# Kernel tuning notes

Measured on AMD Instinct MI355X. Metric: run time of the kernel, lower is better.

The kernel has to match this reference:

```python
import jax, jax.numpy as jnp
import numpy as np

NUM_GRAPHS = 512   # number of graphs in the batch
MAX_NODES = 192    # static pad bound (actual sizes are in [96,160])
TOTAL = 65536      # total atoms across all graphs
D = 256            # model dim (from MultiheadAttention(256, 4))
H = 4              # heads
DH = D // H        # head dim = 64


def setup_inputs() -> dict:
    # Ragged graph sizes that sum exactly to TOTAL (pairs 128+p / 128-p).
    rng = np.random.default_rng(0)
    p = rng.integers(0, 33, size=NUM_GRAPHS // 2)
    sizes = np.concatenate([128 + p, 128 - p])
    rng.shuffle(sizes)
    batch = np.repeat(np.arange(NUM_GRAPHS, dtype=np.int32), sizes)

    key = jax.random.key(0)
    ks = jax.random.split(key, 12)
    s = 0.02
    return {
        "x": jax.random.normal(ks[0], (TOTAL, D), jnp.float32),
        "batch": jnp.asarray(batch),
        # attn1 (torch MultiheadAttention packed in_proj + out_proj)
        "in_w1": jax.random.normal(ks[1], (3 * D, D), jnp.float32) * s,
        "in_b1": jnp.zeros((3 * D,), jnp.float32),
        "out_w1": jax.random.normal(ks[2], (D, D), jnp.float32) * s,
        "out_b1": jnp.zeros((D,), jnp.float32),
        # attn2
        "in_w2": jax.random.normal(ks[3], (3 * D, D), jnp.float32) * s,
        "in_b2": jnp.zeros((3 * D,), jnp.float32),
        "out_w2": jax.random.normal(ks[4], (D, D), jnp.float32) * s,
        "out_b2": jnp.zeros((D,), jnp.float32),
        # readout MLP: 256 -> 256 -> 128 -> 1 (dropout is identity in eval)
        "r_w1": jax.random.normal(ks[5], (256, 256), jnp.float32) * s,
        "r_b1": jnp.zeros((256,), jnp.float32),
        "r_w2": jax.random.normal(ks[6], (128, 256), jnp.float32) * s,
        "r_b2": jnp.zeros((128,), jnp.float32),
        "r_w3": jax.random.normal(ks[7], (1, 128), jnp.float32) * s,
        "r_b3": jnp.zeros((1,), jnp.float32),
    }


def _mha(xd, mask, in_w, in_b, out_w, out_b):
    # xd: [B, L, D], mask: [B, L] (True = valid key). torch MHA semantics.
    B, L, _ = xd.shape
    qkv = xd @ in_w.T + in_b                                  # [B, L, 3D]
    q, k, v = jnp.split(qkv, 3, axis=-1)
    split = lambda t: t.reshape(B, L, H, DH).transpose(0, 2, 1, 3)  # [B,H,L,DH]
    q, k, v = split(q), split(k), split(v)
    scores = jnp.einsum("bhqd,bhkd->bhqk", q, k) / jnp.sqrt(jnp.float32(DH))
    scores = jnp.where(mask[:, None, None, :], scores, -jnp.inf)
    attn = jax.nn.softmax(scores, axis=-1)                    # each graph has >=1 node
    o = jnp.einsum("bhqk,bhkd->bhqd", attn, v)                # [B,H,L,DH]
    o = o.transpose(0, 2, 1, 3).reshape(B, L, D)
    return o @ out_w.T + out_b


def reference(x, batch, in_w1, in_b1, out_w1, out_b1,
              in_w2, in_b2, out_w2, out_b2,
              r_w1, r_b1, r_w2, r_b2, r_w3, r_b3):
    # Scatter ragged atoms into a padded dense [B, MAX_NODES, D] block
    # (equivalent to the per-graph Python loop, but one fused pass).
    idx = jnp.arange(TOTAL)
    pos = idx - jnp.searchsorted(batch, batch, side="left")   # position within graph
    dense = jnp.zeros((NUM_GRAPHS, MAX_NODES, D), x.dtype).at[batch, pos].set(x)
    mask = jnp.zeros((NUM_GRAPHS, MAX_NODES), bool).at[batch, pos].set(True)

    h = _mha(dense, mask, in_w1, in_b1, out_w1, out_b1)
    h = _mha(h, mask, in_w2, in_b2, out_w2, out_b2)

    # masked mean-pool over valid nodes of each graph
    m = mask[..., None].astype(h.dtype)
    pooled = (h * m).sum(axis=1) / m.sum(axis=1)              # [B, D]

    h1 = jax.nn.relu(pooled @ r_w1.T + r_b1)                  # dropout = identity (eval)
    h2 = jax.nn.relu(h1 @ r_w2.T + r_b2)
    energy = h2 @ r_w3.T + r_b3                               # [B, 1]
    return energy[:, 0]                                       # (batch_size,)
```

## Files before the change

kernel.cpp:

```cpp
#include <hip/hip_runtime.h>
#include <math.h>

#define TOTAL 65536
#define NG 512
#define DMODEL 256
#define QKVLD 768

typedef __attribute__((ext_vector_type(8))) short bf16x8;
typedef __attribute__((ext_vector_type(4))) float f32x4;

__device__ inline ushort f2bf(float f) {
    unsigned int u = __float_as_uint(f);
    unsigned int r = (u + 0x7FFFu + ((u >> 16) & 1u)) >> 16;
    return (ushort)r;
}
__device__ inline float bf2f(ushort h) { return __uint_as_float(((unsigned int)h) << 16); }

__device__ __forceinline__ void llds16(const void* gptr, void* lptr) {
    __builtin_amdgcn_global_load_lds(
        (const __attribute__((address_space(1))) unsigned int*)gptr,
        (__attribute__((address_space(3))) unsigned int*)lptr, 16, 0, 0);
}

__global__ __launch_bounds__(256) void prep_kernel(
    const float* __restrict__ x, const float* __restrict__ in_w1,
    const float* __restrict__ in_w2, const float* __restrict__ out_w1,
    const float* __restrict__ out_b1, const float* __restrict__ in_b2,
    const int* __restrict__ batch,
    ushort* __restrict__ xb, ushort* __restrict__ Wb1,
    ushort* __restrict__ Wc2b, float* __restrict__ bc2, int* __restrict__ starts)
{
    const int b = blockIdx.x, t = threadIdx.x;
    if (b < 16384) {
        int i = b * 256 + t;
        float4 v = ((const float4*)x)[i];
        ushort4 u;
        u.x = f2bf(v.x); u.y = f2bf(v.y); u.z = f2bf(v.z); u.w = f2bf(v.w);
        ((ushort4*)xb)[i] = u;
    } else if (b < 16576) {
        int i = (b - 16384) * 256 + t;
        float4 v = ((const float4*)in_w1)[i];
        ushort4 u;
        u.x = f2bf(v.x); u.y = f2bf(v.y); u.z = f2bf(v.z); u.w = f2bf(v.w);
        ((ushort4*)Wb1)[i] = u;
    } else if (b < 17344) {
        const int n = b - 16576;
        __shared__ float wrow[256];
        wrow[t] = in_w2[n * 256 + t];
        __syncthreads();
        float s = 0.f;
#pragma unroll 8
        for (int j = 0; j < 256; ++j) s += wrow[j] * out_w1[j * 256 + t];
        Wc2b[n * 256 + t] = f2bf(s);
    } else if (b < 17347) {
        int n = (b - 17344) * 256 + t;
        if (n < 768) {
            float s = 0.f;
            for (int j = 0; j < 256; ++j) s += in_w2[n * 256 + j] * out_b1[j];
            bc2[n] = s + in_b2[n];
        }
    } else {
        int g = (b - 17347) * 256 + t;
        if (g < NG) {
            int lo = 0, hi = TOTAL;
            while (lo < hi) {
                int mid = (lo + hi) >> 1;
                if (batch[mid] < g) lo = mid + 1; else hi = mid;
            }
            starts[g] = lo;
            if (g == 0) starts[NG] = TOTAL;
        }
    }
}

__global__ __launch_bounds__(256) void gemm_mfma(
    const ushort* __restrict__ A,
    const ushort* __restrict__ W,
    const float* __restrict__ bias,
    ushort* __restrict__ C, int ldc)
{
    __shared__ ushort As[128 * 64];
    __shared__ ushort Bs[128 * 64];
    const int tid = threadIdx.x;
    const int lane = tid & 63, wid = tid >> 6;
    const int grp = lane >> 4, ln16 = lane & 15;
    const int wm = wid & 1, wn = wid >> 1;
    const int n0 = blockIdx.x * 128, m0 = blockIdx.y * 128;

    const int lrow = lane >> 3;
    const int lchunk = (lane & 7) ^ lrow;

    f32x4 acc[4][4];
#pragma unroll
    for (int i = 0; i < 4; ++i)
#pragma unroll
        for (int j = 0; j < 4; ++j) acc[i][j] = (f32x4){0.f, 0.f, 0.f, 0.f};

    for (int k0 = 0; k0 < 256; k0 += 64) {
#pragma unroll
        for (int j = 0; j < 4; ++j) {
            int band = wid * 32 + j * 8;
            int row = band + lrow;
            llds16(A + (size_t)(m0 + row) * 256 + k0 + lchunk * 8, &As[band * 64]);
            llds16(W + (size_t)(n0 + row) * 256 + k0 + lchunk * 8, &Bs[band * 64]);
        }
        __syncthreads();
#pragma unroll
        for (int kc = 0; kc < 2; ++kc) {
            bf16x8 a[4], b[4];
#pragma unroll
            for (int i = 0; i < 4; ++i) {
                int r = wm * 64 + i * 16 + ln16;
                int p = (kc * 4 + grp) ^ (r & 7);
                a[i] = *(const bf16x8*)&As[r * 64 + p * 8];
            }
#pragma unroll
            for (int j = 0; j < 4; ++j) {
                int r = wn * 64 + j * 16 + ln16;
                int p = (kc * 4 + grp) ^ (r & 7);
                b[j] = *(const bf16x8*)&Bs[r * 64 + p * 8];
            }
#pragma unroll
            for (int i = 0; i < 4; ++i)
#pragma unroll
                for (int j = 0; j < 4; ++j)
                    acc[i][j] = __builtin_amdgcn_mfma_f32_16x16x32_bf16(a[i], b[j], acc[i][j], 0, 0, 0);
        }
        __syncthreads();
    }

#pragma unroll
    for (int j = 0; j < 4; ++j) {
        int col = n0 + wn * 64 + j * 16 + ln16;
        float bv = bias[col];
#pragma unroll
        for (int i = 0; i < 4; ++i) {
            int r0 = m0 + wm * 64 + i * 16 + grp * 4;
#pragma unroll
            for (int reg = 0; reg < 4; ++reg)
                C[(size_t)(r0 + reg) * ldc + col] = f2bf(acc[i][j][reg] + bv);
        }
    }
}

#define VLD 168
#define PLD 72

__global__ __launch_bounds__(256) void attn_mfma(const ushort* __restrict__ qkv,
                                                 ushort* __restrict__ obuf,
                                                 float* __restrict__ psumOut,
                                                 const int* __restrict__ starts) {
    __shared__ ushort Ks[160 * 64];
    __shared__ ushort Vt[64 * VLD];
    __shared__ ushort Ps[4 * 16 * PLD];
    __shared__ float  red[4][64];
    const int g = blockIdx.x;
    const int h = blockIdx.y;
    int s = starts[g];
    int e = starts[g + 1];
    s = (s < 0) ? 0 : ((s > TOTAL) ? TOTAL : s);
    e = (e < s) ? s : ((e > TOTAL) ? TOTAL : e);
    int L = e - s;
    if (L > 160) L = 160;
    if (L < 1) L = 1;
    const int tid = threadIdx.x;
    const int lane = tid & 63, wid = tid >> 6;
    const int grp = lane >> 4, ln16 = lane & 15;
    const int lrow = lane >> 3;
    const int lchunk = (lane & 7) ^ lrow;

#pragma unroll
    for (int r = 0; r < 5; ++r) {
        int band = (r * 4 + wid) * 8;
        int row = band + lrow;
        int crow = (row < L) ? row : (L - 1);
        llds16(qkv + (size_t)(s + crow) * QKVLD + 256 + h * 64 + lchunk * 8, &Ks[band * 64]);
    }
#pragma unroll
    for (int r = 0; r < 5; ++r) {
        int idx = r * 256 + tid;
        int kc = idx >> 6;
        int d = idx & 63;
        ushort tmp[8];
#pragma unroll
        for (int j = 0; j < 8; ++j) {
            int key = kc * 8 + j;
            int ckey = (key < L) ? key : (L - 1);
            tmp[j] = qkv[(size_t)(s + ckey) * QKVLD + 512 + h * 64 + d];
        }
        *(uint4*)&Vt[d * VLD + kc * 8] = *(const uint4*)tmp;
    }
    __syncthreads();

    ushort* myP = &Ps[wid * 16 * PLD];
    float psum[4] = {0.f, 0.f, 0.f, 0.f};
    const bool pooled = (psumOut != nullptr);

    for (int q0 = wid * 16; q0 < L; q0 += 64) {
        bf16x8 qa[2];
        {
            int qi = q0 + ln16;
            int grow = (qi < L) ? (s + qi) : s;
            const ushort* qbase = qkv + (size_t)grow * QKVLD + h * 64;
            qa[0] = *(const bf16x8*)(qbase + grp * 8);
            qa[1] = *(const bf16x8*)(qbase + 32 + grp * 8);
        }
        f32x4 sc[10];
#pragma unroll
        for (int kt = 0; kt < 10; ++kt) {
            int row = kt * 16 + ln16;
            int p0 = grp ^ (row & 7);
            int p1 = (4 + grp) ^ (row & 7);
            bf16x8 b0 = *(const bf16x8*)&Ks[row * 64 + p0 * 8];
            bf16x8 b1 = *(const bf16x8*)&Ks[row * 64 + p1 * 8];
            f32x4 z = (f32x4){0.f, 0.f, 0.f, 0.f};
            z = __builtin_amdgcn_mfma_f32_16x16x32_bf16(qa[0], b0, z, 0, 0, 0);
            z = __builtin_amdgcn_mfma_f32_16x16x32_bf16(qa[1], b1, z, 0, 0, 0);
            sc[kt] = z;
        }
        float sm[4] = {0.f, 0.f, 0.f, 0.f};
#pragma unroll
        for (int kt = 0; kt < 10; ++kt) {
            bool dead = (kt * 16 + ln16) >= L;
#pragma unroll
            for (int r = 0; r < 4; ++r) {
                float p = __expf(dead ? -INFINITY : sc[kt][r] * 0.125f);
                sc[kt][r] = p;
                sm[r] += p;
            }
        }
#pragma unroll
        for (int m = 1; m <= 8; m <<= 1)
#pragma unroll
            for (int r = 0; r < 4; ++r) sm[r] += __shfl_xor(sm[r], m, 64);
        float inv[4];
#pragma unroll
        for (int r = 0; r < 4; ++r) inv[r] = 1.f / sm[r];

        f32x4 o[4];
#pragma unroll
        for (int dt = 0; dt < 4; ++dt) o[dt] = (f32x4){0.f, 0.f, 0.f, 0.f};
#pragma unroll
        for (int st = 0; st < 3; ++st) {
            const int nkt = (st == 2) ? 2 : 4;
            const int nkc = (st == 2) ? 1 : 2;
#pragma unroll
            for (int kti = 0; kti < 4; ++kti) {
                if (kti < nkt) {
                    int kt = st * 4 + kti;
#pragma unroll
                    for (int r = 0; r < 4; ++r)
                        myP[(grp * 4 + r) * PLD + kti * 16 + ln16] = f2bf(sc[kt][r]);
                }
            }
#pragma unroll
            for (int kc2 = 0; kc2 < 2; ++kc2) {
                if (kc2 < nkc) {
                    bf16x8 pa = *(const bf16x8*)&myP[ln16 * PLD + kc2 * 32 + grp * 8];
                    int kcg = st * 2 + kc2;
#pragma unroll
                    for (int dt = 0; dt < 4; ++dt) {
                        bf16x8 vb = *(const bf16x8*)&Vt[(dt * 16 + ln16) * VLD + kcg * 32 + grp * 8];
                        o[dt] = __builtin_amdgcn_mfma_f32_16x16x32_bf16(pa, vb, o[dt], 0, 0, 0);
                    }
                }
            }
        }
        if (pooled) {
#pragma unroll
            for (int dt = 0; dt < 4; ++dt)
#pragma unroll
                for (int reg = 0; reg < 4; ++reg) {
                    int q = q0 + grp * 4 + reg;
                    if (q < L) psum[dt] += o[dt][reg] * inv[reg];
                }
        } else {
#pragma unroll
            for (int dt = 0; dt < 4; ++dt)
#pragma unroll
                for (int reg = 0; reg < 4; ++reg) {
                    int q = q0 + grp * 4 + reg;
                    if (q < L)
                        obuf[(size_t)(s + q) * DMODEL + h * 64 + dt * 16 + ln16] =
                            f2bf(o[dt][reg] * inv[reg]);
                }
        }
    }

    if (pooled) {
#pragma unroll
        for (int dt = 0; dt < 4; ++dt) {
            psum[dt] += __shfl_xor(psum[dt], 16, 64);
            psum[dt] += __shfl_xor(psum[dt], 32, 64);
        }
        if (grp == 0) {
#pragma unroll
            for (int dt = 0; dt < 4; ++dt) red[wid][dt * 16 + ln16] = psum[dt];
        }
        __syncthreads();
        if (tid < 64) {
            float v = red[0][tid] + red[1][tid] + red[2][tid] + red[3][tid];
            psumOut[g * DMODEL + h * 64 + tid] = v;
        }
    }
}

__global__ __launch_bounds__(256) void readout_kernel(
    const float* __restrict__ psum, const int* __restrict__ starts,
    const float* __restrict__ ow2, const float* __restrict__ ob2,
    const float* __restrict__ w1, const float* __restrict__ b1,
    const float* __restrict__ w2, const float* __restrict__ b2,
    const float* __restrict__ w3, const float* __restrict__ b3,
    float* __restrict__ out)
{
    __shared__ float xs[256], ps[256], h1s[256], h2s[128];
    const int g = blockIdx.x, t = threadIdx.x;
    int s = starts[g], e = starts[g + 1];
    s = (s < 0) ? 0 : ((s > TOTAL) ? TOTAL : s);
    e = (e < s) ? s : ((e > TOTAL) ? TOTAL : e);
    int L = e - s;
    if (L < 1) L = 1;
    xs[t] = psum[g * 256 + t] / (float)L;
    __syncthreads();
    {
        const float* wr = ow2 + t * 256;
        float s0 = 0.f;
#pragma unroll 8
        for (int i = 0; i < 256; ++i) s0 += xs[i] * wr[i];
        ps[t] = s0 + ob2[t];
    }
    __syncthreads();
    {
        const float* wr = w1 + t * 256;
        float s0 = 0.f;
#pragma unroll 8
        for (int i = 0; i < 256; ++i) s0 += ps[i] * wr[i];
        float v = s0 + b1[t];
        h1s[t] = v > 0.f ? v : 0.f;
    }
    __syncthreads();
    if (t < 128) {
        const float* wr = w2 + t * 256;
        float s0 = 0.f;
#pragma unroll 8
        for (int i = 0; i < 256; ++i) s0 += h1s[i] * wr[i];
        float v = s0 + b2[t];
        h2s[t] = v > 0.f ? v : 0.f;
    }
    __syncthreads();
    if (t < 64) {
        float v = h2s[t] * w3[t] + h2s[t + 64] * w3[t + 64];
#pragma unroll
        for (int off = 32; off > 0; off >>= 1) v += __shfl_down(v, off, 64);
        if (t == 0) out[g] = v + b3[0];
    }
}

__global__ __launch_bounds__(256) void zero_out_kernel(float* __restrict__ out, int n) {
    int i = blockIdx.x * 256 + threadIdx.x;
    if (i < n) out[i] = 0.f;
}

extern "C" void kernel_launch(void* const* d_in, const int* in_sizes, int n_in,
                              void* d_out, int out_size, void* d_ws, size_t ws_size,
                              hipStream_t stream) {
    float* out = (float*)d_out;

    const int expect[16] = {
        TOTAL * DMODEL, TOTAL,
        3 * DMODEL * DMODEL, 3 * DMODEL,
        DMODEL * DMODEL, DMODEL,
        3 * DMODEL * DMODEL, 3 * DMODEL,
        DMODEL * DMODEL, DMODEL,
        256 * 256, 256,
        128 * 256, 128,
        128, 1
    };
    const size_t NEEDED = 135536640ull;
    bool ok = (n_in == 16) && (out_size == NG) && (d_ws != nullptr) && (ws_size >= NEEDED);
    if (ok) {
        for (int i = 0; i < 16; ++i)
            if (in_sizes[i] != expect[i]) { ok = false; break; }
    }
    if (!ok) {
        zero_out_kernel<<<(out_size + 255) / 256, 256, 0, stream>>>(out, out_size);
        return;
    }

    const float* x      = (const float*)d_in[0];
    const int*   batch  = (const int*)d_in[1];
    const float* in_w1  = (const float*)d_in[2];
    const float* in_b1  = (const float*)d_in[3];
    const float* out_w1 = (const float*)d_in[4];
    const float* out_b1 = (const float*)d_in[5];
    const float* in_w2  = (const float*)d_in[6];
    const float* in_b2  = (const float*)d_in[7];
    const float* out_w2 = (const float*)d_in[8];
    const float* out_b2 = (const float*)d_in[9];
    const float* r_w1   = (const float*)d_in[10];
    const float* r_b1   = (const float*)d_in[11];
    const float* r_w2   = (const float*)d_in[12];
    const float* r_b2   = (const float*)d_in[13];
    const float* r_w3   = (const float*)d_in[14];
    const float* r_b3   = (const float*)d_in[15];

    char* ws = (char*)d_ws;
    int*    starts = (int*)(ws + 0);
    float*  bc2    = (float*)(ws + 4096);
    float*  psum   = (float*)(ws + 8192);
    ushort* Wc2b   = (ushort*)(ws + 532480);
    ushort* Wb1    = (ushort*)(ws + 925696);
    ushort* bufO   = (ushort*)(ws + 1318912);
    ushort* bufQKV = (ushort*)(ws + 34873344ull);

    prep_kernel<<<17349, 256, 0, stream>>>(x, in_w1, in_w2, out_w1, out_b1, in_b2,
                                           batch, bufO, Wb1, Wc2b, bc2, starts);

    gemm_mfma<<<dim3(6, 512), 256, 0, stream>>>(bufO, Wb1, in_b1, bufQKV, QKVLD);
    attn_mfma<<<dim3(NG, 4), 256, 0, stream>>>(bufQKV, bufO, nullptr, starts);

    gemm_mfma<<<dim3(6, 512), 256, 0, stream>>>(bufO, Wc2b, bc2, bufQKV, QKVLD);
    attn_mfma<<<dim3(NG, 4), 256, 0, stream>>>(bufQKV, bufO, psum, starts);

    readout_kernel<<<NG, 256, 0, stream>>>(psum, starts, out_w2, out_b2,
                                           r_w1, r_b1, r_w2, r_b2, r_w3, r_b3, out);
}
```

Baseline: 377.0 us.

## Fuse QKV projection GEMM into per-graph attention kernel

Replaces the separate QKV GEMM and attention kernels with one kernel per (graph, head). It computes the head's Q, K and V projections from the input rows in shared memory and then runs attention directly. This removes the QKV intermediate buffer's global write and read and cuts the number of launches. In exchange, each block recomputes projections on a small tile (at most 160 rows) with less data reuse, uses more shared memory per block, and the phases are serialized inside the block.

```diff
diff --git a/kernel.cpp b/kernel.cpp
--- a/kernel.cpp
+++ b/kernel.cpp
@@ -73,87 +73,17 @@
     }
 }
 
-__global__ __launch_bounds__(256) void gemm_mfma(
-    const ushort* __restrict__ A,
+#define VLD 168
+
+__global__ __launch_bounds__(256) void fused_layer(
+    const ushort* __restrict__ X,
     const ushort* __restrict__ W,
     const float* __restrict__ bias,
-    ushort* __restrict__ C, int ldc)
+    ushort* __restrict__ obuf,
+    float* __restrict__ psumOut,
+    const int* __restrict__ starts)
 {
-    __shared__ ushort As[128 * 64];
-    __shared__ ushort Bs[128 * 64];
-    const int tid = threadIdx.x;
-    const int lane = tid & 63, wid = tid >> 6;
-    const int grp = lane >> 4, ln16 = lane & 15;
-    const int wm = wid & 1, wn = wid >> 1;
-    const int n0 = blockIdx.x * 128, m0 = blockIdx.y * 128;
-
-    const int lrow = lane >> 3;
-    const int lchunk = (lane & 7) ^ lrow;
-
-    f32x4 acc[4][4];
-#pragma unroll
-    for (int i = 0; i < 4; ++i)
-#pragma unroll
-        for (int j = 0; j < 4; ++j) acc[i][j] = (f32x4){0.f, 0.f, 0.f, 0.f};
-
-    for (int k0 = 0; k0 < 256; k0 += 64) {
-#pragma unroll
-        for (int j = 0; j < 4; ++j) {
-            int band = wid * 32 + j * 8;
-            int row = band + lrow;
-            llds16(A + (size_t)(m0 + row) * 256 + k0 + lchunk * 8, &As[band * 64]);
-            llds16(W + (size_t)(n0 + row) * 256 + k0 + lchunk * 8, &Bs[band * 64]);
-        }
-        __syncthreads();
-#pragma unroll
-        for (int kc = 0; kc < 2; ++kc) {
-            bf16x8 a[4], b[4];
-#pragma unroll
-            for (int i = 0; i < 4; ++i) {
-                int r = wm * 64 + i * 16 + ln16;
-                int p = (kc * 4 + grp) ^ (r & 7);
-                a[i] = *(const bf16x8*)&As[r * 64 + p * 8];
-            }
-#pragma unroll
-            for (int j = 0; j < 4; ++j) {
-                int r = wn * 64 + j * 16 + ln16;
-                int p = (kc * 4 + grp) ^ (r & 7);
-                b[j] = *(const bf16x8*)&Bs[r * 64 + p * 8];
-            }
-#pragma unroll
-            for (int i = 0; i < 4; ++i)
-#pragma unroll
-                for (int j = 0; j < 4; ++j)
-                    acc[i][j] = __builtin_amdgcn_mfma_f32_16x16x32_bf16(a[i], b[j], acc[i][j], 0, 0, 0);
-        }
-        __syncthreads();
-    }
-
-#pragma unroll
-    for (int j = 0; j < 4; ++j) {
-        int col = n0 + wn * 64 + j * 16 + ln16;
-        float bv = bias[col];
-#pragma unroll
-        for (int i = 0; i < 4; ++i) {
-            int r0 = m0 + wm * 64 + i * 16 + grp * 4;
-#pragma unroll
-            for (int reg = 0; reg < 4; ++reg)
-                C[(size_t)(r0 + reg) * ldc + col] = f2bf(acc[i][j][reg] + bv);
-        }
-    }
-}
-
-#define VLD 168
-#define PLD 72
-
-__global__ __launch_bounds__(256) void attn_mfma(const ushort* __restrict__ qkv,
-                                                 ushort* __restrict__ obuf,
-                                                 float* __restrict__ psumOut,
-                                                 const int* __restrict__ starts) {
-    __shared__ ushort Ks[160 * 64];
-    __shared__ ushort Vt[64 * VLD];
-    __shared__ ushort Ps[4 * 16 * PLD];
-    __shared__ float  red[4][64];
+    __shared__ __align__(16) ushort smem[26112];
     const int g = blockIdx.x;
     const int h = blockIdx.y;
     int s = starts[g];
@@ -166,128 +96,249 @@
     const int tid = threadIdx.x;
     const int lane = tid & 63, wid = tid >> 6;
     const int grp = lane >> 4, ln16 = lane & 15;
-    const int lrow = lane >> 3;
-    const int lchunk = (lane & 7) ^ lrow;
-
-#pragma unroll
-    for (int r = 0; r < 5; ++r) {
-        int band = (r * 4 + wid) * 8;
-        int row = band + lrow;
-        int crow = (row < L) ? row : (L - 1);
-        llds16(qkv + (size_t)(s + crow) * QKVLD + 256 + h * 64 + lchunk * 8, &Ks[band * 64]);
-    }
-#pragma unroll
-    for (int r = 0; r < 5; ++r) {
-        int idx = r * 256 + tid;
-        int kc = idx >> 6;
-        int d = idx & 63;
-        ushort tmp[8];
-#pragma unroll
-        for (int j = 0; j < 8; ++j) {
-            int key = kc * 8 + j;
-            int ckey = (key < L) ? key : (L - 1);
-            tmp[j] = qkv[(size_t)(s + ckey) * QKVLD + 512 + h * 64 + d];
-        }
-        *(uint4*)&Vt[d * VLD + kc * 8] = *(const uint4*)tmp;
-    }
+    const int lrow8 = lane >> 3;
+    const int lxor = (lane & 7) ^ lrow8;
+    const int nt = (wid < 2) ? 3 : 2;
+    const int mt0 = (wid < 2) ? wid * 3 : 6 + (wid - 2) * 2;
+    const int Sw = 20992 + wid * 1152;
+
+    float bq[4], bk[4], bv2[2];
+#pragma unroll
+    for (int j = 0; j < 4; ++j) {
+        bq[j] = bias[h * 64 + j * 16 + ln16];
+        bk[j] = bias[256 + h * 64 + j * 16 + ln16];
+    }
+    const int wm = wid & 1, wn = wid >> 1;
+#pragma unroll
+    for (int j = 0; j < 2; ++j)
+        bv2[j] = bias[512 + h * 64 + wn * 32 + j * 16 + ln16];
+
+    f32x4 acc[3][8];
+#pragma unroll
+    for (int t = 0; t < 3; ++t)
+#pragma unroll
+        for (int j = 0; j < 8; ++j) acc[t][j] = (f32x4){0.f, 0.f, 0.f, 0.f};
+
+    for (int c = 0; c < 4; ++c) {
+#pragma unroll
+        for (int r = 0; r < 5; ++r) {
+            int band = wid * 5 + r;
+            int row = band * 8 + lrow8;
+            int crow = (row < L) ? row : (L - 1);
+            llds16(X + (size_t)(s + crow) * 256 + c * 64 + lxor * 8, &smem[band * 512]);
+        }
+#pragma unroll
+        for (int r = 0; r < 4; ++r) {
+            int band = wid * 4 + r;
+            int gg = band * 8 + lrow8;
+            int wrow = (gg < 64) ? (h * 64 + gg) : (256 + h * 64 + (gg - 64));
+            llds16(W + (size_t)wrow * 256 + c * 64 + lxor * 8, &smem[10240 + band * 512]);
+        }
+        __syncthreads();
+#pragma unroll
+        for (int kc = 0; kc < 2; ++kc) {
+            bf16x8 a[3], bb[8];
+#pragma unroll
+            for (int t = 0; t < 3; ++t) {
+                if (t < nt) {
+                    int row = (mt0 + t) * 16 + ln16;
+                    a[t] = *(const bf16x8*)&smem[row * 64 + (((kc * 4 + grp) ^ (row & 7)) * 8)];
+                }
+            }
+#pragma unroll
+            for (int j = 0; j < 8; ++j) {
+                int col = j * 16 + ln16;
+                bb[j] = *(const bf16x8*)&smem[10240 + col * 64 + (((kc * 4 + grp) ^ (col & 7)) * 8)];
+            }
+#pragma unroll
+            for (int t = 0; t < 3; ++t) {
+                if (t < nt) {
+#pragma unroll
+                    for (int j = 0; j < 8; ++j)
+                        acc[t][j] = __builtin_amdgcn_mfma_f32_16x16x32_bf16(a[t], bb[j], acc[t][j], 0, 0, 0);
+                }
+            }
+        }
+        __syncthreads();
+    }
+#pragma unroll
+    for (int t = 0; t < 3; ++t) {
+        if (t < nt) {
+#pragma unroll
+            for (int j = 0; j < 4; ++j) {
+                int d = j * 16 + ln16;
+#pragma unroll
+                for (int reg = 0; reg < 4; ++reg) {
+                    int key = (mt0 + t) * 16 + grp * 4 + reg;
+                    smem[key * 64 + (((d >> 3) ^ (key & 7)) * 8) + (d & 7)] =
+                        f2bf(acc[t][4 + j][reg] + bk[j]);
+                }
+            }
+        }
+    }
+
+    f32x4 accv[5][2];
+#pragma unroll
+    for (int i = 0; i < 5; ++i)
+#pragma unroll
+        for (int j = 0; j < 2; ++j) accv[i][j] = (f32x4){0.f, 0.f, 0.f, 0.f};
+
+    for (int c = 0; c < 4; ++c) {
+#pragma unroll
+        for (int r = 0; r < 5; ++r) {
+            int band = wid * 5 + r;
+            int row = band * 8 + lrow8;
+            int crow = (row < L) ? row : (L - 1);
+            llds16(X + (size_t)(s + crow) * 256 + c * 64 + lxor * 8, &smem[10240 + band * 512]);
+        }
+#pragma unroll
+        for (int r = 0; r < 2; ++r) {
+            int band = wid * 2 + r;
+            int gg = band * 8 + lrow8;
+            llds16(W + (size_t)(512 + h * 64 + gg) * 256 + c * 64 + lxor * 8,
+                   &smem[20992 + band * 512]);
+        }
+        __syncthreads();
+#pragma unroll
+        for (int kc = 0; kc < 2; ++kc) {
+            bf16x8 av[5], bv[2];
+#pragma unroll
+            for (int i = 0; i < 5; ++i) {
+                int row = (wm * 5 + i) * 16 + ln16;
+                av[i] = *(const bf16x8*)&smem[10240 + row * 64 + (((kc * 4 + grp) ^ (row & 7)) * 8)];
+            }
+#pragma unroll
+            for (int j = 0; j < 2; ++j) {
+                int col = wn * 32 + j * 16 + ln16;
+                bv[j] = *(const bf16x8*)&smem[20992 + col * 64 + (((kc * 4 + grp) ^ (col & 7)) * 8)];
+            }
+#pragma unroll
+            for (int i = 0; i < 5; ++i)
+#pragma unroll
+                for (int j = 0; j < 2; ++j)
+                    accv[i][j] = __builtin_amdgcn_mfma_f32_16x16x32_bf16(av[i], bv[j], accv[i][j], 0, 0, 0);
+        }
+        __syncthreads();
+    }
+#pragma unroll
+    for (int i = 0; i < 5; ++i)
+#pragma unroll
+        for (int j = 0; j < 2; ++j) {
+            int d = wn * 32 + j * 16 + ln16;
+            int keybase = wm * 80 + i * 16 + grp * 4;
+            ushort4 pk;
+            pk.x = f2bf(accv[i][j][0] + bv2[j]);
+            pk.y = f2bf(accv[i][j][1] + bv2[j]);
+            pk.z = f2bf(accv[i][j][2] + bv2[j]);
+            pk.w = f2bf(accv[i][j][3] + bv2[j]);
+            *(ushort4*)&smem[10240 + d * VLD + keybase] = pk;
+        }
     __syncthreads();
 
-    ushort* myP = &Ps[wid * 16 * PLD];
     float psum[4] = {0.f, 0.f, 0.f, 0.f};
     const bool pooled = (psumOut != nullptr);
 
-    for (int q0 = wid * 16; q0 < L; q0 += 64) {
-        bf16x8 qa[2];
-        {
-            int qi = q0 + ln16;
-            int grow = (qi < L) ? (s + qi) : s;
-            const ushort* qbase = qkv + (size_t)grow * QKVLD + h * 64;
-            qa[0] = *(const bf16x8*)(qbase + grp * 8);
-            qa[1] = *(const bf16x8*)(qbase + 32 + grp * 8);
-        }
-        f32x4 sc[10];
-#pragma unroll
-        for (int kt = 0; kt < 10; ++kt) {
-            int row = kt * 16 + ln16;
-            int p0 = grp ^ (row & 7);
-            int p1 = (4 + grp) ^ (row & 7);
-            bf16x8 b0 = *(const bf16x8*)&Ks[row * 64 + p0 * 8];
-            bf16x8 b1 = *(const bf16x8*)&Ks[row * 64 + p1 * 8];
-            f32x4 z = (f32x4){0.f, 0.f, 0.f, 0.f};
-            z = __builtin_amdgcn_mfma_f32_16x16x32_bf16(qa[0], b0, z, 0, 0, 0);
-            z = __builtin_amdgcn_mfma_f32_16x16x32_bf16(qa[1], b1, z, 0, 0, 0);
-            sc[kt] = z;
-        }
-        float sm[4] = {0.f, 0.f, 0.f, 0.f};
-#pragma unroll
-        for (int kt = 0; kt < 10; ++kt) {
-            bool dead = (kt * 16 + ln16) >= L;
-#pragma unroll
-            for (int r = 0; r < 4; ++r) {
-                float p = __expf(dead ? -INFINITY : sc[kt][r] * 0.125f);
-                sc[kt][r] = p;
-                sm[r] += p;
-            }
-        }
-#pragma unroll
-        for (int m = 1; m <= 8; m <<= 1)
-#pragma unroll
-            for (int r = 0; r < 4; ++r) sm[r] += __shfl_xor(sm[r], m, 64);
-        float inv[4];
-#pragma unroll
-        for (int r = 0; r < 4; ++r) inv[r] = 1.f / sm[r];
-
-        f32x4 o[4];
-#pragma unroll
-        for (int dt = 0; dt < 4; ++dt) o[dt] = (f32x4){0.f, 0.f, 0.f, 0.f};
-#pragma unroll
-        for (int st = 0; st < 3; ++st) {
-            const int nkt = (st == 2) ? 2 : 4;
-            const int nkc = (st == 2) ? 1 : 2;
-#pragma unroll
-            for (int kti = 0; kti < 4; ++kti) {
-                if (kti < nkt) {
-                    int kt = st * 4 + kti;
-#pragma unroll
-                    for (int r = 0; r < 4; ++r)
-                        myP[(grp * 4 + r) * PLD + kti * 16 + ln16] = f2bf(sc[kt][r]);
-                }
-            }
-#pragma unroll
-            for (int kc2 = 0; kc2 < 2; ++kc2) {
-                if (kc2 < nkc) {
-                    bf16x8 pa = *(const bf16x8*)&myP[ln16 * PLD + kc2 * 32 + grp * 8];
-                    int kcg = st * 2 + kc2;
-#pragma unroll
-                    for (int dt = 0; dt < 4; ++dt) {
-                        bf16x8 vb = *(const bf16x8*)&Vt[(dt * 16 + ln16) * VLD + kcg * 32 + grp * 8];
-                        o[dt] = __builtin_amdgcn_mfma_f32_16x16x32_bf16(pa, vb, o[dt], 0, 0, 0);
+#pragma unroll
+    for (int t = 0; t < 3; ++t) {
+        if (t < nt) {
+            int q0 = (mt0 + t) * 16;
+            if (q0 < L) {
+#pragma unroll
+                for (int j = 0; j < 4; ++j)
+#pragma unroll
+                    for (int reg = 0; reg < 4; ++reg) {
+                        int q = grp * 4 + reg;
+                        int d = j * 16 + ln16;
+                        smem[Sw + q * 64 + (((d >> 3) ^ (q & 7)) * 8) + (d & 7)] =
+                            f2bf(acc[t][j][reg] + bq[j]);
                     }
-                }
-            }
-        }
-        if (pooled) {
-#pragma unroll
-            for (int dt = 0; dt < 4; ++dt)
-#pragma unroll
-                for (int reg = 0; reg < 4; ++reg) {
-                    int q = q0 + grp * 4 + reg;
-                    if (q < L) psum[dt] += o[dt][reg] * inv[reg];
-                }
-        } else {
-#pragma unroll
-            for (int dt = 0; dt < 4; ++dt)
-#pragma unroll
-                for (int reg = 0; reg < 4; ++reg) {
-                    int q = q0 + grp * 4 + reg;
-                    if (q < L)
-                        obuf[(size_t)(s + q) * DMODEL + h * 64 + dt * 16 + ln16] =
-                            f2bf(o[dt][reg] * inv[reg]);
-                }
+                bf16x8 qa0 = *(const bf16x8*)&smem[Sw + ln16 * 64 + ((grp ^ (ln16 & 7)) * 8)];
+                bf16x8 qa1 = *(const bf16x8*)&smem[Sw + ln16 * 64 + (((4 + grp) ^ (ln16 & 7)) * 8)];
+
+                f32x4 sc[10];
+#pragma unroll
+                for (int kt = 0; kt < 10; ++kt) {
+                    int row = kt * 16 + ln16;
+                    bf16x8 b0 = *(const bf16x8*)&smem[row * 64 + ((grp ^ (row & 7)) * 8)];
+                    bf16x8 b1 = *(const bf16x8*)&smem[row * 64 + (((4 + grp) ^ (row & 7)) * 8)];
+                    f32x4 z = (f32x4){0.f, 0.f, 0.f, 0.f};
+                    z = __builtin_amdgcn_mfma_f32_16x16x32_bf16(qa0, b0, z, 0, 0, 0);
+                    z = __builtin_amdgcn_mfma_f32_16x16x32_bf16(qa1, b1, z, 0, 0, 0);
+                    sc[kt] = z;
+                }
+                float sm[4] = {0.f, 0.f, 0.f, 0.f};
+#pragma unroll
+                for (int kt = 0; kt < 10; ++kt) {
+                    bool dead = (kt * 16 + ln16) >= L;
+#pragma unroll
+                    for (int r = 0; r < 4; ++r) {
+                        float p = __expf(dead ? -INFINITY : sc[kt][r] * 0.125f);
+                        sc[kt][r] = p;
+                        sm[r] += p;
+                    }
+                }
+#pragma unroll
+                for (int m = 1; m <= 8; m <<= 1)
+#pragma unroll
+                    for (int r = 0; r < 4; ++r) sm[r] += __shfl_xor(sm[r], m, 64);
+                float inv[4];
+#pragma unroll
+                for (int r = 0; r < 4; ++r) inv[r] = 1.f / sm[r];
+
+                f32x4 o[4];
+#pragma unroll
+                for (int dt = 0; dt < 4; ++dt) o[dt] = (f32x4){0.f, 0.f, 0.f, 0.f};
+#pragma unroll
+                for (int st = 0; st < 3; ++st) {
+                    const int nkt = (st == 2) ? 2 : 4;
+                    const int nkc = (st == 2) ? 1 : 2;
+#pragma unroll
+                    for (int kti = 0; kti < 4; ++kti) {
+                        if (kti < nkt) {
+                            int kt = st * 4 + kti;
+#pragma unroll
+                            for (int r = 0; r < 4; ++r)
+                                smem[Sw + (grp * 4 + r) * 72 + kti * 16 + ln16] = f2bf(sc[kt][r]);
+                        }
+                    }
+#pragma unroll
+                    for (int kc2 = 0; kc2 < 2; ++kc2) {
+                        if (kc2 < nkc) {
+                            bf16x8 pa = *(const bf16x8*)&smem[Sw + ln16 * 72 + kc2 * 32 + grp * 8];
+                            int kcg = st * 2 + kc2;
+#pragma unroll
+                            for (int dt = 0; dt < 4; ++dt) {
+                                bf16x8 vb = *(const bf16x8*)&smem[10240 + (dt * 16 + ln16) * VLD + kcg * 32 + grp * 8];
+                                o[dt] = __builtin_amdgcn_mfma_f32_16x16x32_bf16(pa, vb, o[dt], 0, 0, 0);
+                            }
+                        }
+                    }
+                }
+                if (pooled) {
+#pragma unroll
+                    for (int dt = 0; dt < 4; ++dt)
+#pragma unroll
+                        for (int reg = 0; reg < 4; ++reg) {
+                            int q = q0 + grp * 4 + reg;
+                            if (q < L) psum[dt] += o[dt][reg] * inv[reg];
+                        }
+                } else {
+#pragma unroll
+                    for (int dt = 0; dt < 4; ++dt)
+#pragma unroll
+                        for (int reg = 0; reg < 4; ++reg) {
+                            int q = q0 + grp * 4 + reg;
+                            if (q < L)
+                                obuf[(size_t)(s + q) * DMODEL + h * 64 + dt * 16 + ln16] =
+                                    f2bf(o[dt][reg] * inv[reg]);
+                        }
+                }
+            }
         }
     }
 
     if (pooled) {
+        float* redf = (float*)&smem[25600];
 #pragma unroll
         for (int dt = 0; dt < 4; ++dt) {
             psum[dt] += __shfl_xor(psum[dt], 16, 64);
@@ -295,11 +346,11 @@
         }
         if (grp == 0) {
 #pragma unroll
-            for (int dt = 0; dt < 4; ++dt) red[wid][dt * 16 + ln16] = psum[dt];
+            for (int dt = 0; dt < 4; ++dt) redf[wid * 64 + dt * 16 + ln16] = psum[dt];
         }
         __syncthreads();
         if (tid < 64) {
-            float v = red[0][tid] + red[1][tid] + red[2][tid] + red[3][tid];
+            float v = redf[tid] + redf[64 + tid] + redf[128 + tid] + redf[192 + tid];
             psumOut[g * DMODEL + h * 64 + tid] = v;
         }
     }
@@ -410,17 +461,14 @@
     float*  psum   = (float*)(ws + 8192);
     ushort* Wc2b   = (ushort*)(ws + 532480);
     ushort* Wb1    = (ushort*)(ws + 925696);
-    ushort* bufO   = (ushort*)(ws + 1318912);
-    ushort* bufQKV = (ushort*)(ws + 34873344ull);
+    ushort* xb     = (ushort*)(ws + 1318912);
+    ushort* bufO1  = (ushort*)(ws + 34873344ull);
 
     prep_kernel<<<17349, 256, 0, stream>>>(x, in_w1, in_w2, out_w1, out_b1, in_b2,
-                                           batch, bufO, Wb1, Wc2b, bc2, starts);
-
-    gemm_mfma<<<dim3(6, 512), 256, 0, stream>>>(bufO, Wb1, in_b1, bufQKV, QKVLD);
-    attn_mfma<<<dim3(NG, 4), 256, 0, stream>>>(bufQKV, bufO, nullptr, starts);
-
-    gemm_mfma<<<dim3(6, 512), 256, 0, stream>>>(bufO, Wc2b, bc2, bufQKV, QKVLD);
-    attn_mfma<<<dim3(NG, 4), 256, 0, stream>>>(bufQKV, bufO, psum, starts);
+                                           batch, xb, Wb1, Wc2b, bc2, starts);
+
+    fused_layer<<<dim3(NG, 4), 256, 0, stream>>>(xb, Wb1, in_b1, bufO1, nullptr, starts);
+    fused_layer<<<dim3(NG, 4), 256, 0, stream>>>(bufO1, Wc2b, bc2, nullptr, psum, starts);
 
     readout_kernel<<<NG, 256, 0, stream>>>(psum, starts, out_w2, out_b2,
                                            r_w1, r_b1, r_w2, r_b2, r_w3, r_b3, out);
```

Result: slower. 450.6 us (+19.5%).

## Fuse all stages into one persistent cooperative kernel with grid syncs

Applied to the files above, without the earlier changes.

Refactors the prep, QKV GEMM, attention and readout kernels into device functions and runs them as job loops inside a single cooperative mega-kernel of 768 blocks separated by grid-wide syncs. This removes the separate kernel launches and inter-kernel gaps. It adds grid barrier costs, caps occupancy at three blocks per CU with shared memory sized for the largest stage, and may worsen load balance. A fallback to the original multi-launch path runs if the cooperative launch fails.

```diff
diff --git a/kernel.cpp b/kernel.cpp
--- a/kernel.cpp
+++ b/kernel.cpp
@@ -1,10 +1,15 @@
 #include <hip/hip_runtime.h>
+#include <hip/hip_cooperative_groups.h>
 #include <math.h>
+
+namespace cg = cooperative_groups;
 
 #define TOTAL 65536
 #define NG 512
 #define DMODEL 256
 #define QKVLD 768
+#define VLD 168
+#define PLD 72
 
 typedef __attribute__((ext_vector_type(8))) short bf16x8;
 typedef __attribute__((ext_vector_type(4))) float f32x4;
@@ -22,15 +27,17 @@
         (__attribute__((address_space(3))) unsigned int*)lptr, 16, 0, 0);
 }
 
-__global__ __launch_bounds__(256) void prep_kernel(
+
+__device__ __forceinline__ void prep_job(
+    int b, int t,
     const float* __restrict__ x, const float* __restrict__ in_w1,
     const float* __restrict__ in_w2, const float* __restrict__ out_w1,
     const float* __restrict__ out_b1, const float* __restrict__ in_b2,
     const int* __restrict__ batch,
     ushort* __restrict__ xb, ushort* __restrict__ Wb1,
-    ushort* __restrict__ Wc2b, float* __restrict__ bc2, int* __restrict__ starts)
-{
-    const int b = blockIdx.x, t = threadIdx.x;
+    ushort* __restrict__ Wc2b, float* __restrict__ bc2, int* __restrict__ starts,
+    float* wrow)
+{
     if (b < 16384) {
         int i = b * 256 + t;
         float4 v = ((const float4*)x)[i];
@@ -45,13 +52,13 @@
         ((ushort4*)Wb1)[i] = u;
     } else if (b < 17344) {
         const int n = b - 16576;
-        __shared__ float wrow[256];
         wrow[t] = in_w2[n * 256 + t];
         __syncthreads();
         float s = 0.f;
 #pragma unroll 8
         for (int j = 0; j < 256; ++j) s += wrow[j] * out_w1[j * 256 + t];
         Wc2b[n * 256 + t] = f2bf(s);
+        __syncthreads();
     } else if (b < 17347) {
         int n = (b - 17344) * 256 + t;
         if (n < 768) {
@@ -73,20 +80,14 @@
     }
 }
 
-__global__ __launch_bounds__(256) void gemm_mfma(
-    const ushort* __restrict__ A,
-    const ushort* __restrict__ W,
-    const float* __restrict__ bias,
-    ushort* __restrict__ C, int ldc)
-{
-    __shared__ ushort As[128 * 64];
-    __shared__ ushort Bs[128 * 64];
-    const int tid = threadIdx.x;
+__device__ __forceinline__ void gemm_tile(
+    const ushort* __restrict__ A, const ushort* __restrict__ W,
+    const float* __restrict__ bias, ushort* __restrict__ C, int ldc,
+    int m0, int n0, ushort* As, ushort* Bs, int tid)
+{
     const int lane = tid & 63, wid = tid >> 6;
     const int grp = lane >> 4, ln16 = lane & 15;
     const int wm = wid & 1, wn = wid >> 1;
-    const int n0 = blockIdx.x * 128, m0 = blockIdx.y * 128;
-
     const int lrow = lane >> 3;
     const int lchunk = (lane & 7) ^ lrow;
 
@@ -143,19 +144,16 @@
     }
 }
 
-#define VLD 168
-#define PLD 72
-
-__global__ __launch_bounds__(256) void attn_mfma(const ushort* __restrict__ qkv,
-                                                 ushort* __restrict__ obuf,
-                                                 float* __restrict__ psumOut,
-                                                 const int* __restrict__ starts) {
-    __shared__ ushort Ks[160 * 64];
-    __shared__ ushort Vt[64 * VLD];
-    __shared__ ushort Ps[4 * 16 * PLD];
-    __shared__ float  red[4][64];
-    const int g = blockIdx.x;
-    const int h = blockIdx.y;
+__device__ __forceinline__ void attn_tile(
+    const ushort* __restrict__ qkv, ushort* __restrict__ obuf,
+    float* __restrict__ psumOut, const int* __restrict__ starts,
+    int g, int h, ushort* smem, int tid)
+{
+    ushort* Ks = smem;
+    ushort* Vt = smem + 10240;
+    ushort* Ps = smem + 20992;
+    float*  red = (float*)(smem + 25600);
+
     int s = starts[g];
     int e = starts[g + 1];
     s = (s < 0) ? 0 : ((s > TOTAL) ? TOTAL : s);
@@ -163,11 +161,12 @@
     int L = e - s;
     if (L > 160) L = 160;
     if (L < 1) L = 1;
-    const int tid = threadIdx.x;
     const int lane = tid & 63, wid = tid >> 6;
     const int grp = lane >> 4, ln16 = lane & 15;
     const int lrow = lane >> 3;
     const int lchunk = (lane & 7) ^ lrow;
+
+    __syncthreads();
 
 #pragma unroll
     for (int r = 0; r < 5; ++r) {
@@ -295,26 +294,28 @@
         }
         if (grp == 0) {
 #pragma unroll
-            for (int dt = 0; dt < 4; ++dt) red[wid][dt * 16 + ln16] = psum[dt];
+            for (int dt = 0; dt < 4; ++dt) red[wid * 64 + dt * 16 + ln16] = psum[dt];
         }
         __syncthreads();
         if (tid < 64) {
-            float v = red[0][tid] + red[1][tid] + red[2][tid] + red[3][tid];
+            float v = red[tid] + red[64 + tid] + red[128 + tid] + red[192 + tid];
             psumOut[g * DMODEL + h * 64 + tid] = v;
         }
     }
 }
 
-__global__ __launch_bounds__(256) void readout_kernel(
-    const float* __restrict__ psum, const int* __restrict__ starts,
+__device__ __forceinline__ void readout_tile(
+    int g, int t, const float* __restrict__ psum, const int* __restrict__ starts,
     const float* __restrict__ ow2, const float* __restrict__ ob2,
     const float* __restrict__ w1, const float* __restrict__ b1,
     const float* __restrict__ w2, const float* __restrict__ b2,
     const float* __restrict__ w3, const float* __restrict__ b3,
-    float* __restrict__ out)
-{
-    __shared__ float xs[256], ps[256], h1s[256], h2s[128];
-    const int g = blockIdx.x, t = threadIdx.x;
+    float* __restrict__ out, float* sm)
+{
+    float* xs = sm;
+    float* ps = sm + 256;
+    float* h1s = sm + 512;
+    float* h2s = sm + 768;
     int s = starts[g], e = starts[g + 1];
     s = (s < 0) ? 0 : ((s > TOTAL) ? TOTAL : s);
     e = (e < s) ? s : ((e > TOTAL) ? TOTAL : e);
@@ -354,6 +355,91 @@
         for (int off = 32; off > 0; off >>= 1) v += __shfl_down(v, off, 64);
         if (t == 0) out[g] = v + b3[0];
     }
+}
+
+struct MegaArgs {
+    const float* x; const int* batch;
+    const float* in_w1; const float* in_b1;
+    const float* out_w1; const float* out_b1;
+    const float* in_w2; const float* in_b2;
+    const float* out_w2; const float* out_b2;
+    const float* r_w1; const float* r_b1;
+    const float* r_w2; const float* r_b2;
+    const float* r_w3; const float* r_b3;
+    ushort* xbO;
+    ushort* Wb1; ushort* Wc2b; float* bc2;
+    int* starts; float* psum;
+    ushort* bufQKV;
+    float* out;
+};
+
+__global__ __launch_bounds__(256, 3) void mega_kernel(MegaArgs a) {
+    __shared__ __align__(16) ushort smem[26112];
+    cg::grid_group gridg = cg::this_grid();
+    const int t = threadIdx.x;
+    const int nb = gridDim.x;
+
+    for (int job = blockIdx.x; job < 17349; job += nb)
+        prep_job(job, t, a.x, a.in_w1, a.in_w2, a.out_w1, a.out_b1, a.in_b2, a.batch,
+                 a.xbO, a.Wb1, a.Wc2b, a.bc2, a.starts, (float*)smem);
+    gridg.sync();
+
+    for (int job = blockIdx.x; job < 3072; job += nb)
+        gemm_tile(a.xbO, a.Wb1, a.in_b1, a.bufQKV, QKVLD,
+                  (job / 6) * 128, (job % 6) * 128, smem, smem + 8192, t);
+    gridg.sync();
+
+    for (int job = blockIdx.x; job < 2048; job += nb)
+        attn_tile(a.bufQKV, a.xbO, nullptr, a.starts, job >> 2, job & 3, smem, t);
+    gridg.sync();
+
+    for (int job = blockIdx.x; job < 3072; job += nb)
+        gemm_tile(a.xbO, a.Wc2b, a.bc2, a.bufQKV, QKVLD,
+                  (job / 6) * 128, (job % 6) * 128, smem, smem + 8192, t);
+    gridg.sync();
+
+    for (int job = blockIdx.x; job < 2048; job += nb)
+        attn_tile(a.bufQKV, nullptr, a.psum, a.starts, job >> 2, job & 3, smem, t);
+    gridg.sync();
+
+    for (int job = blockIdx.x; job < 512; job += nb)
+        readout_tile(job, t, a.psum, a.starts, a.out_w2, a.out_b2,
+                     a.r_w1, a.r_b1, a.r_w2, a.r_b2, a.r_w3, a.r_b3, a.out, (float*)smem);
+}
+
+__global__ __launch_bounds__(256) void prep_kernel(
+    const float* x, const float* in_w1, const float* in_w2, const float* out_w1,
+    const float* out_b1, const float* in_b2, const int* batch,
+    ushort* xb, ushort* Wb1, ushort* Wc2b, float* bc2, int* starts)
+{
+    __shared__ float wrow[256];
+    prep_job(blockIdx.x, threadIdx.x, x, in_w1, in_w2, out_w1, out_b1, in_b2, batch,
+             xb, Wb1, Wc2b, bc2, starts, wrow);
+}
+
+__global__ __launch_bounds__(256) void gemm_mfma(
+    const ushort* A, const ushort* W, const float* bias, ushort* C, int ldc)
+{
+    __shared__ __align__(16) ushort sm[16384];
+    gemm_tile(A, W, bias, C, ldc, blockIdx.y * 128, blockIdx.x * 128,
+              sm, sm + 8192, threadIdx.x);
+}
+
+__global__ __launch_bounds__(256) void attn_mfma(
+    const ushort* qkv, ushort* obuf, float* psumOut, const int* starts)
+{
+    __shared__ __align__(16) ushort sm[26112];
+    attn_tile(qkv, obuf, psumOut, starts, blockIdx.x, blockIdx.y, sm, threadIdx.x);
+}
+
+__global__ __launch_bounds__(256) void readout_kernel(
+    const float* psum, const int* starts,
+    const float* ow2, const float* ob2, const float* w1, const float* b1,
+    const float* w2, const float* b2, const float* w3, const float* b3, float* out)
+{
+    __shared__ float sm[896];
+    readout_tile(blockIdx.x, threadIdx.x, psum, starts, ow2, ob2, w1, b1, w2, b2,
+                 w3, b3, out, sm);
 }
 
 __global__ __launch_bounds__(256) void zero_out_kernel(float* __restrict__ out, int n) {
@@ -410,18 +496,36 @@
     float*  psum   = (float*)(ws + 8192);
     ushort* Wc2b   = (ushort*)(ws + 532480);
     ushort* Wb1    = (ushort*)(ws + 925696);
-    ushort* bufO   = (ushort*)(ws + 1318912);
+    ushort* xbO    = (ushort*)(ws + 1318912);
     ushort* bufQKV = (ushort*)(ws + 34873344ull);
 
-    prep_kernel<<<17349, 256, 0, stream>>>(x, in_w1, in_w2, out_w1, out_b1, in_b2,
-                                           batch, bufO, Wb1, Wc2b, bc2, starts);
-
-    gemm_mfma<<<dim3(6, 512), 256, 0, stream>>>(bufO, Wb1, in_b1, bufQKV, QKVLD);
-    attn_mfma<<<dim3(NG, 4), 256, 0, stream>>>(bufQKV, bufO, nullptr, starts);
-
-    gemm_mfma<<<dim3(6, 512), 256, 0, stream>>>(bufO, Wc2b, bc2, bufQKV, QKVLD);
-    attn_mfma<<<dim3(NG, 4), 256, 0, stream>>>(bufQKV, bufO, psum, starts);
-
-    readout_kernel<<<NG, 256, 0, stream>>>(psum, starts, out_w2, out_b2,
-                                           r_w1, r_b1, r_w2, r_b2, r_w3, r_b3, out);
-}
+    MegaArgs a;
+    a.x = x; a.batch = batch;
+    a.in_w1 = in_w1; a.in_b1 = in_b1;
+    a.out_w1 = out_w1; a.out_b1 = out_b1;
+    a.in_w2 = in_w2; a.in_b2 = in_b2;
+    a.out_w2 = out_w2; a.out_b2 = out_b2;
+    a.r_w1 = r_w1; a.r_b1 = r_b1;
+    a.r_w2 = r_w2; a.r_b2 = r_b2;
+    a.r_w3 = r_w3; a.r_b3 = r_b3;
+    a.xbO = xbO; a.Wb1 = Wb1; a.Wc2b = Wc2b; a.bc2 = bc2;
+    a.starts = starts; a.psum = psum;
+    a.bufQKV = bufQKV;
+    a.out = out;
+
+    void* kparams[] = { (void*)&a };
+    hipError_t cerr = hipLaunchCooperativeKernel((const void*)mega_kernel,
+                                                 dim3(768), dim3(256),
+                                                 kparams, 0u, stream);
+    if (cerr != hipSuccess) {
+        (void)hipGetLastError();
+        prep_kernel<<<17349, 256, 0, stream>>>(x, in_w1, in_w2, out_w1, out_b1, in_b2,
+                                               batch, xbO, Wb1, Wc2b, bc2, starts);
+        gemm_mfma<<<dim3(6, 512), 256, 0, stream>>>(xbO, Wb1, in_b1, bufQKV, QKVLD);
+        attn_mfma<<<dim3(NG, 4), 256, 0, stream>>>(bufQKV, xbO, nullptr, starts);
+        gemm_mfma<<<dim3(6, 512), 256, 0, stream>>>(xbO, Wc2b, bc2, bufQKV, QKVLD);
+        attn_mfma<<<dim3(NG, 4), 256, 0, stream>>>(bufQKV, nullptr, psum, starts);
+        readout_kernel<<<NG, 256, 0, stream>>>(psum, starts, out_w2, out_b2,
+                                               r_w1, r_b1, r_w2, r_b2, r_w3, r_b3, out);
+    }
+}
```

Result: slower. 880.7 us (+133.6%).
